# Kernel tuning notes

Hardware: AMD Instinct MI355X
Metric: run time of the kernel (lower is better)

Reference implementation:

```python
import jax, jax.numpy as jnp
import numpy as np

B, S, HID = 1, 4096, 2048
NH, NKV, HD, RD = 16, 4, 128, 64
EPS = 1e-6
SCALE = HD ** -0.5


def _rmsnorm(x, w, eps=EPS):
    x32 = x.astype(jnp.float32)
    var = jnp.mean(x32 * x32, axis=-1, keepdims=True)
    return (w * (x32 * jax.lax.rsqrt(var + eps))).astype(x.dtype)


def _rotate_half(x):
    x1, x2 = jnp.split(x, 2, axis=-1)
    return jnp.concatenate([-x2, x1], axis=-1)


def setup_inputs() -> dict:
    key = jax.random.key(0)
    ks = jax.random.split(key, 6)
    hidden_states = jax.random.normal(ks[0], (B, S, HID), dtype=jnp.float32)
    # real rotary embeddings for rotary_dim=RD
    inv_freq = 1.0 / (10000.0 ** (jnp.arange(0, RD, 2, dtype=jnp.float32) / RD))
    pos = jnp.arange(S, dtype=jnp.float32)
    freqs = pos[:, None] * inv_freq[None, :]          # [S, RD/2]
    emb = jnp.concatenate([freqs, freqs], axis=-1)     # [S, RD]
    cos = jnp.cos(emb)[None]                           # [1, S, RD]
    sin = jnp.sin(emb)[None]
    w = 0.02
    Wq = jax.random.normal(ks[1], (NH * HD, HID), dtype=jnp.float32) * w
    Wk = jax.random.normal(ks[2], (NKV * HD, HID), dtype=jnp.float32) * w
    Wv = jax.random.normal(ks[3], (NKV * HD, HID), dtype=jnp.float32) * w
    Wo = jax.random.normal(ks[4], (HID, NH * HD), dtype=jnp.float32) * w
    q_norm_w = jnp.ones((NH * HD,), dtype=jnp.float32)
    k_norm_w = jnp.ones((NKV * HD,), dtype=jnp.float32)
    return {"hidden_states": hidden_states, "cos": cos, "sin": sin,
            "Wq": Wq, "Wk": Wk, "Wv": Wv, "Wo": Wo,
            "q_norm_w": q_norm_w, "k_norm_w": k_norm_w}


def _attention(hidden_states, cos, sin, Wq, Wk, Wv, Wo, q_norm_w, k_norm_w):
    bsz, q_len, _ = hidden_states.shape
    q = hidden_states @ Wq.T                 # [B,S,NH*HD]
    k = hidden_states @ Wk.T                 # [B,S,NKV*HD]
    v = hidden_states @ Wv.T
    q = _rmsnorm(q, q_norm_w)
    k = _rmsnorm(k, k_norm_w)
    q = q.reshape(bsz, q_len, NH, HD).transpose(0, 2, 1, 3)   # b h s d
    k = k.reshape(bsz, q_len, NKV, HD).transpose(0, 2, 1, 3)
    v = v.reshape(bsz, q_len, NKV, HD).transpose(0, 2, 1, 3)
    # partial RoPE on first RD dims
    c = cos[:, None]  # [B,1,S,RD]
    s = sin[:, None]
    q_rot, q_pass = q[..., :RD], q[..., RD:]
    k_rot, k_pass = k[..., :RD], k[..., RD:]
    q = jnp.concatenate([q_rot * c + _rotate_half(q_rot) * s, q_pass], axis=-1)
    k = jnp.concatenate([k_rot * c + _rotate_half(k_rot) * s, k_pass], axis=-1)
    # GQA: repeat kv heads
    n_rep = NH // NKV
    k = jnp.repeat(k, n_rep, axis=1)
    v = jnp.repeat(v, n_rep, axis=1)
    scores = jnp.einsum('bhqd,bhkd->bhqk', q, k) * SCALE
    causal = jnp.triu(jnp.full((q_len, q_len), -jnp.inf, dtype=scores.dtype), k=1)
    scores = scores + causal
    probs = jax.nn.softmax(scores.astype(jnp.float32), axis=-1).astype(q.dtype)
    out = jnp.einsum('bhqk,bhkd->bhqd', probs, v)
    out = out.transpose(0, 2, 1, 3).reshape(bsz, q_len, NH * HD)
    return out @ Wo.T


def reference(hidden_states, cos, sin, Wq, Wk, Wv, Wo, q_norm_w, k_norm_w):
    return _attention(hidden_states, cos, sin, Wq, Wk, Wv, Wo, q_norm_w, k_norm_w)
```

## Files before the change

### kernel.cpp

```cpp
#include <hip/hip_runtime.h>

typedef unsigned short u16;
typedef unsigned int   u32;
typedef __bf16 bf16x8 __attribute__((ext_vector_type(8)));
typedef float  f32x4  __attribute__((ext_vector_type(4)));

#define S_LEN 4096
#define HIDN  2048
#define NHEAD 16
#define NKVH  4
#define HDIM  128
#define ROTD  64
#define QKVN  3072

__device__ __forceinline__ u16 f2bf(float f) {
  union { float f; u32 u; } v; v.f = f;
  u32 r = v.u + 0x7FFFu + ((v.u >> 16) & 1u);
  return (u16)(r >> 16);
}
__device__ __forceinline__ u16 f2bf_fast(float f) {
  union { __bf16 b; u16 u; } cv; cv.b = (__bf16)f; return cv.u;
}
__device__ __forceinline__ float bf2f(u16 u) {
  union { u32 u; float f; } v; v.u = ((u32)u) << 16; return v.f;
}
__device__ __forceinline__ void gl2lds16(const u16* g, u16* l) {
  __builtin_amdgcn_global_load_lds((const __attribute__((address_space(1))) void*)g,
                                   (__attribute__((address_space(3))) void*)l, 16, 0, 0);
}
__device__ __forceinline__ f32x4 mfma_bf16(bf16x8 a, bf16x8 b, f32x4 c) {
  return __builtin_amdgcn_mfma_f32_16x16x32_bf16(a, b, c, 0, 0, 0);
}
template <int N> __device__ __forceinline__ void vmwait() {
  if constexpr (N == 7)      asm volatile("s_waitcnt vmcnt(7)" ::: "memory");
  else if constexpr (N == 6) asm volatile("s_waitcnt vmcnt(6)" ::: "memory");
  else                       asm volatile("s_waitcnt vmcnt(0)" ::: "memory");
}

__global__ __launch_bounds__(256) void cvt_f32_bf16(const float* __restrict__ in,
                                                    u16* __restrict__ out) {
  size_t i = ((size_t)blockIdx.x * 256 + threadIdx.x) * 8;
  float4 a = *(const float4*)(in + i);
  float4 b = *(const float4*)(in + i + 4);
  uint4 r;
  r.x = (u32)f2bf(a.x) | ((u32)f2bf(a.y) << 16);
  r.y = (u32)f2bf(a.z) | ((u32)f2bf(a.w) << 16);
  r.z = (u32)f2bf(b.x) | ((u32)f2bf(b.y) << 16);
  r.w = (u32)f2bf(b.z) | ((u32)f2bf(b.w) << 16);
  *(uint4*)(out + i) = r;
}

template <int BN, int NB, bool BF16OUT>
__global__ __launch_bounds__(512, 2) void gemm_big(const u16* __restrict__ A,
                                                   const u16* __restrict__ Bm,
                                                   void* __restrict__ Cp,
                                                   int M, int N, int K) {
  constexpr int WNC = BN / 4;
  constexpr int NF  = WNC / 16;
  constexpr int ASZ = 256 * 128;
  constexpr int BUF = ASZ + BN * 128;
  constexpr int LOADS = 4 + NB;
  __shared__ __align__(1024) char lds[2 * BUF];

  const int tid = threadIdx.x, wave = tid >> 6, lane = tid & 63;
  const int wm = wave >> 2, wn = wave & 3;
  const int row0 = blockIdx.x * 256, col0 = blockIdx.y * BN;
  const int l8 = lane >> 3, l7 = lane & 7;
  const int T = K >> 6;

  const u16* gA[4]; const u16* gB[NB];
  u16* ldsA[4]; u16* ldsB[NB];
  #pragma unroll
  for (int i = 0; i < 4; ++i) {
    gA[i]  = A + (size_t)(row0 + wave * 32 + i * 8 + l8) * K + (l7 ^ l8) * 8;
    ldsA[i] = (u16*)(lds + wave * 4096 + i * 1024);
  }
  #pragma unroll
  for (int i = 0; i < NB; ++i) {
    gB[i]  = Bm + (size_t)(col0 + wave * (BN / 8) + i * 8 + l8) * K + (l7 ^ l8) * 8;
    ldsB[i] = (u16*)(lds + ASZ + wave * (BN * 16) + i * 1024);
  }
  auto stage = [&](int buf, int t) {
    const size_t ko = (size_t)t * 64;
    #pragma unroll
    for (int i = 0; i < 4; ++i)
      gl2lds16(gA[i] + ko, (u16*)((char*)ldsA[i] + buf * BUF));
    #pragma unroll
    for (int i = 0; i < NB; ++i)
      gl2lds16(gB[i] + ko, (u16*)((char*)ldsB[i] + buf * BUF));
  };

  const int colx0 = (((lane >> 4))     ^ l7) * 16;
  const int colx1 = ((4 + (lane >> 4)) ^ l7) * 16;
  const char* aB = lds + (wm * 128 + (lane & 15)) * 128;
  const char* bB = lds + ASZ + (wn * WNC + (lane & 15)) * 128;

  f32x4 acc[8][NF];
  #pragma unroll
  for (int i = 0; i < 8; ++i)
    #pragma unroll
    for (int j = 0; j < NF; ++j) { f32x4 z = {0.f,0.f,0.f,0.f}; acc[i][j] = z; }

  stage(0, 0);
  stage(1, 1);
  vmwait<LOADS>();
  __builtin_amdgcn_s_barrier();

  for (int t = 0; t < T; ++t) {
    const int bo = (t & 1) * BUF;
    #pragma unroll
    for (int kh = 0; kh < 2; ++kh) {
      const int cx = kh ? colx1 : colx0;
      bf16x8 bfr[NF];
      #pragma unroll
      for (int nf = 0; nf < NF; ++nf)
        bfr[nf] = *(const bf16x8*)(bB + bo + nf * 2048 + cx);
      #pragma unroll
      for (int mh = 0; mh < 2; ++mh) {
        bf16x8 af[4];
        #pragma unroll
        for (int mf = 0; mf < 4; ++mf)
          af[mf] = *(const bf16x8*)(aB + bo + mh * 8192 + mf * 2048 + cx);
        __builtin_amdgcn_s_setprio(1);
        #pragma unroll
        for (int mf = 0; mf < 4; ++mf)
          #pragma unroll
          for (int nf = 0; nf < NF; ++nf)
            acc[mh * 4 + mf][nf] = mfma_bf16(af[mf], bfr[nf], acc[mh * 4 + mf][nf]);
        __builtin_amdgcn_s_setprio(0);
      }
    }
    asm volatile("s_waitcnt lgkmcnt(0)" ::: "memory");
    __builtin_amdgcn_s_barrier();
    if (t + 2 < T) stage(t & 1, t + 2);
    if (t + 1 < T) {
      if (t + 2 < T) vmwait<LOADS>();
      else           vmwait<0>();
      __builtin_amdgcn_s_barrier();
    }
  }

  const int mwv = row0 + wm * 128, nwv = col0 + wn * WNC;
  #pragma unroll
  for (int mf8 = 0; mf8 < 8; ++mf8)
    #pragma unroll
    for (int nf = 0; nf < NF; ++nf)
      #pragma unroll
      for (int r = 0; r < 4; ++r) {
        int m = mwv + (mf8 >> 2) * 64 + (mf8 & 3) * 16 + (lane >> 4) * 4 + r;
        int n = nwv + nf * 16 + (lane & 15);
        float v = acc[mf8][nf][r];
        if (BF16OUT) ((u16*)Cp)[(size_t)m * N + n] = f2bf(v);
        else         ((float*)Cp)[(size_t)m * N + n] = v;
      }
}

__global__ __launch_bounds__(256) void norm_rope(const u16* __restrict__ qkv,
                                                 const float* __restrict__ cosb,
                                                 const float* __restrict__ sinb,
                                                 const float* __restrict__ qw,
                                                 const float* __restrict__ kw,
                                                 u16* __restrict__ Qo,
                                                 u16* __restrict__ Ko) {
  const int s = blockIdx.x, t = threadIdx.x;
  const int wave = t >> 6, lane = t & 63;
  const float SL = 0.08838834764831845f * 1.4426950408889634f;
  __shared__ float rowbuf[HIDN];
  __shared__ float red[4];
  const u16* base = qkv + (size_t)s * QKVN;

  float x[8];
  {
    uint4 v = *(const uint4*)(base + t * 8);
    u32 w4[4] = {v.x, v.y, v.z, v.w};
    #pragma unroll
    for (int j = 0; j < 4; ++j) {
      x[2*j]   = bf2f((u16)(w4[j] & 0xffffu));
      x[2*j+1] = bf2f((u16)(w4[j] >> 16));
    }
  }
  float ss = 0.f;
  #pragma unroll
  for (int j = 0; j < 8; ++j) ss += x[j] * x[j];
  #pragma unroll
  for (int m = 1; m < 64; m <<= 1) ss += __shfl_xor(ss, m);
  if (lane == 0) red[wave] = ss;
  __syncthreads();
  float rs = rsqrtf((red[0]+red[1]+red[2]+red[3]) * (1.0f / HIDN) + 1e-6f);
  #pragma unroll
  for (int j = 0; j < 8; ++j) rowbuf[t*8 + j] = x[j] * rs * qw[t*8 + j];
  __syncthreads();
  {
    int i0 = t * 8, d0 = i0 & (HDIM - 1), hh = i0 >> 7;
    float o[8];
    if (d0 < ROTD) {
      #pragma unroll
      for (int j = 0; j < 8; ++j) {
        int d = d0 + j;
        float rot = (d < 32) ? -rowbuf[i0 + j + 32] : rowbuf[i0 + j - 32];
        o[j] = rowbuf[i0 + j] * cosb[s*ROTD + d] + rot * sinb[s*ROTD + d];
      }
    } else {
      #pragma unroll
      for (int j = 0; j < 8; ++j) o[j] = rowbuf[i0 + j];
    }
    uint4 r;
    r.x = (u32)f2bf(o[0]*SL) | ((u32)f2bf(o[1]*SL) << 16);
    r.y = (u32)f2bf(o[2]*SL) | ((u32)f2bf(o[3]*SL) << 16);
    r.z = (u32)f2bf(o[4]*SL) | ((u32)f2bf(o[5]*SL) << 16);
    r.w = (u32)f2bf(o[6]*SL) | ((u32)f2bf(o[7]*SL) << 16);
    *(uint4*)(Qo + ((size_t)hh * S_LEN + s) * HDIM + d0) = r;
  }

  const u16* kbase = base + HIDN;
  float y0, y1;
  { u32 v = *(const u32*)(kbase + t * 2); y0 = bf2f((u16)(v & 0xffffu)); y1 = bf2f((u16)(v >> 16)); }
  float ss2 = y0*y0 + y1*y1;
  #pragma unroll
  for (int m = 1; m < 64; m <<= 1) ss2 += __shfl_xor(ss2, m);
  __syncthreads();
  if (lane == 0) red[wave] = ss2;
  __syncthreads();
  float rs2 = rsqrtf((red[0]+red[1]+red[2]+red[3]) * (1.0f / 512.0f) + 1e-6f);
  rowbuf[t*2]     = y0 * rs2 * kw[t*2];
  rowbuf[t*2 + 1] = y1 * rs2 * kw[t*2 + 1];
  __syncthreads();
  {
    int i0 = t * 2, d0 = i0 & (HDIM - 1), hh = i0 >> 7;
    float o0, o1;
    if (d0 < ROTD) {
      float r0 = (d0 < 32) ? -rowbuf[i0 + 32] : rowbuf[i0 - 32];
      float r1 = (d0 + 1 < 32) ? -rowbuf[i0 + 1 + 32] : rowbuf[i0 + 1 - 32];
      o0 = rowbuf[i0]     * cosb[s*ROTD + d0]     + r0 * sinb[s*ROTD + d0];
      o1 = rowbuf[i0 + 1] * cosb[s*ROTD + d0 + 1] + r1 * sinb[s*ROTD + d0 + 1];
    } else { o0 = rowbuf[i0]; o1 = rowbuf[i0 + 1]; }
    u32 r = (u32)f2bf(o0) | ((u32)f2bf(o1) << 16);
    *(u32*)(Ko + ((size_t)hh * S_LEN + s) * HDIM + d0) = r;
  }
}

__global__ __launch_bounds__(256) void vtrans(const u16* __restrict__ qkv,
                                              u16* __restrict__ Vt) {
  const int sb = blockIdx.x * 64, db = blockIdx.y * 64, kvh = blockIdx.z;
  __shared__ u16 tile[64][72];
  const int t = threadIdx.x;
  {
    int r = t >> 2, cc = (t & 3) * 16;
    const u16* src = qkv + (size_t)(sb + r) * QKVN + 2560 + kvh * HDIM + db + cc;
    *(uint4*)&tile[r][cc]     = *(const uint4*)(src);
    *(uint4*)&tile[r][cc + 8] = *(const uint4*)(src + 8);
  }
  __syncthreads();
  {
    int d = t >> 2, sc = (t & 3) * 16;
    u16 tmp[16];
    #pragma unroll
    for (int j = 0; j < 16; ++j) tmp[j] = tile[sc + j][d];
    u16* dst = Vt + ((size_t)kvh * HDIM + db + d) * S_LEN + sb + sc;
    *(uint4*)dst       = *(uint4*)&tmp[0];
    *(uint4*)(dst + 8) = *(uint4*)&tmp[8];
  }
}

__global__ __launch_bounds__(256, 2) void attn_fwd(const u16* __restrict__ Q,
                                                   const u16* __restrict__ K,
                                                   const u16* __restrict__ Vt,
                                                   u16* __restrict__ O) {
  const int bid  = blockIdx.x;
  const int slot = bid & 7, p = bid >> 3;
  const int kvh  = slot >> 1, hp = slot & 1;
  const int tid = threadIdx.x, wave = tid >> 6, lane = tid & 63;
  const int h  = kvh * 4 + hp * 2 + (wave >> 1);
  const int wq = wave & 1;
  __shared__ u16 Ks[2][64][128];
  __shared__ u16 Vs[2][128][64];
  __shared__ u16 Ps[4][32][64];

  const u16* gKb[4]; const u16* gVb[4];
  #pragma unroll
  for (int i = 0; i < 4; ++i) {
    int cc = wave * 4 + i;
    int rk = cc * 4 + (lane >> 4);
    gKb[i] = K + ((size_t)kvh * S_LEN + rk) * HDIM + ((lane & 15) ^ (rk & 7)) * 8;
    int rv = cc * 8 + (lane >> 3);
    gVb[i] = Vt + ((size_t)kvh * HDIM + rv) * S_LEN + ((lane & 7) ^ (rv & 7)) * 8;
  }
  auto stage = [&](int buf, int kvb) {
    #pragma unroll
    for (int i = 0; i < 4; ++i) {
      int cc = wave * 4 + i;
      gl2lds16(gKb[i] + (size_t)kvb * HDIM, &Ks[buf][cc * 4][0]);
      gl2lds16(gVb[i] + kvb,                &Vs[buf][cc * 8][0]);
    }
  };

  int offv[4];
  #pragma unroll
  for (int kk = 0; kk < 4; ++kk)
    offv[kk] = (kk * 64 + (lane >> 4) * 16) ^ ((lane & 7) << 4);
  const char* ksB = (const char*)Ks + (lane & 15) * 256;
  const char* vsB = (const char*)Vs + (lane & 15) * 128;
  const char* psB = (const char*)Ps + wave * 4096 + (lane & 15) * 128;
  char*       pwB = (char*)Ps + wave * 4096;
  const int   lx2 = (lane & 15) * 2;

  stage(0, 0);
  __syncthreads();
  int cur = 0;

  for (int job = 0; job < 2; ++job) {
    const int qb = job ? (63 - p) : p;
    const int ntiles = qb + 1;
    const int qg0 = qb * 64 + wq * 32 + (lane >> 4) * 4;

    bf16x8 qf[2][4];
    #pragma unroll
    for (int qm = 0; qm < 2; ++qm) {
      const u16* qptr = Q + ((size_t)h * S_LEN + qb * 64 + wq * 32 + qm * 16 + (lane & 15)) * HDIM
                        + (lane >> 4) * 8;
      #pragma unroll
      for (int kk = 0; kk < 4; ++kk) qf[qm][kk] = *(const bf16x8*)(qptr + kk * 32);
    }

    float lsum[2][4];
    #pragma unroll
    for (int qm = 0; qm < 2; ++qm)
      #pragma unroll
      for (int r = 0; r < 4; ++r) lsum[qm][r] = 0.f;
    f32x4 o[2][8];
    #pragma unroll
    for (int qm = 0; qm < 2; ++qm)
      #pragma unroll
      for (int i = 0; i < 8; ++i) { f32x4 z = {0.f,0.f,0.f,0.f}; o[qm][i] = z; }

    for (int kt = 0; kt < ntiles; ++kt) {
      if (kt + 1 < ntiles)      stage(cur ^ 1, (kt + 1) * 64);
      else if (job == 0)        stage(cur ^ 1, 0);

      const int bufo = cur << 14;

      f32x4 sc[2][4];
      #pragma unroll
      for (int qm = 0; qm < 2; ++qm)
        #pragma unroll
        for (int i = 0; i < 4; ++i) { f32x4 z = {0.f,0.f,0.f,0.f}; sc[qm][i] = z; }
      __builtin_amdgcn_s_setprio(1);
      #pragma unroll
      for (int kk = 0; kk < 4; ++kk)
        #pragma unroll
        for (int nf = 0; nf < 4; ++nf) {
          bf16x8 kf = *(const bf16x8*)(ksB + bufo + nf * 4096 + offv[kk]);
          sc[0][nf] = mfma_bf16(qf[0][kk], kf, sc[0][nf]);
          sc[1][nf] = mfma_bf16(qf[1][kk], kf, sc[1][nf]);
        }
      __builtin_amdgcn_s_setprio(0);

      if (kt == ntiles - 1) {
        const int kvb = kt * 64;
        #pragma unroll
        for (int qm = 0; qm < 2; ++qm)
          #pragma unroll
          for (int nf = 0; nf < 4; ++nf) {
            int col = kvb + nf * 16 + (lane & 15);
            #pragma unroll
            for (int r = 0; r < 4; ++r) {
              float e = __builtin_amdgcn_exp2f(sc[qm][nf][r]);
              e = (col <= qg0 + qm * 16 + r) ? e : 0.f;
              sc[qm][nf][r] = e;
              lsum[qm][r] += e;
            }
          }
      } else {
        #pragma unroll
        for (int qm = 0; qm < 2; ++qm)
          #pragma unroll
          for (int nf = 0; nf < 4; ++nf)
            #pragma unroll
            for (int r = 0; r < 4; ++r) {
              float e = __builtin_amdgcn_exp2f(sc[qm][nf][r]);
              sc[qm][nf][r] = e;
              lsum[qm][r] += e;
            }
      }

      #pragma unroll
      for (int qm = 0; qm < 2; ++qm)
        #pragma unroll
        for (int nf = 0; nf < 4; ++nf)
          #pragma unroll
          for (int r = 0; r < 4; ++r) {
            int prow = qm * 16 + (lane >> 4) * 4 + r;
            int bcol = (nf * 32 + lx2) ^ ((prow & 7) << 4);
            *(u16*)(pwB + prow * 128 + bcol) = f2bf_fast(sc[qm][nf][r]);
          }

      __builtin_amdgcn_s_setprio(1);
      #pragma unroll
      for (int ks = 0; ks < 2; ++ks) {
        bf16x8 pf0 = *(const bf16x8*)(psB + offv[ks]);
        bf16x8 pf1 = *(const bf16x8*)(psB + 2048 + offv[ks]);
        #pragma unroll
        for (int nf2 = 0; nf2 < 8; ++nf2) {
          bf16x8 vf = *(const bf16x8*)(vsB + bufo + nf2 * 2048 + offv[ks]);
          o[0][nf2] = mfma_bf16(pf0, vf, o[0][nf2]);
          o[1][nf2] = mfma_bf16(pf1, vf, o[1][nf2]);
        }
      }
      __builtin_amdgcn_s_setprio(0);

      __syncthreads();
      cur ^= 1;
    }

    #pragma unroll
    for (int qm = 0; qm < 2; ++qm)
      #pragma unroll
      for (int r = 0; r < 4; ++r) {
        float lt = lsum[qm][r];
        #pragma unroll
        for (int m = 1; m < 16; m <<= 1) lt += __shfl_xor(lt, m);
        float inv = 1.f / lt;
        int srow = qg0 + qm * 16 + r;
        #pragma unroll
        for (int nf2 = 0; nf2 < 8; ++nf2) {
          int col = h * HDIM + nf2 * 16 + (lane & 15);
          O[(size_t)srow * HIDN + col] = f2bf_fast(o[qm][nf2][r] * inv);
        }
      }
  }
}

extern "C" void kernel_launch(void* const* d_in, const int* in_sizes, int n_in,
                              void* d_out, int out_size, void* d_ws, size_t ws_size,
                              hipStream_t stream) {
  (void)in_sizes; (void)n_in; (void)out_size; (void)ws_size;
  const float* h    = (const float*)d_in[0];
  const float* cosb = (const float*)d_in[1];
  const float* sinb = (const float*)d_in[2];
  const float* Wq   = (const float*)d_in[3];
  const float* Wk   = (const float*)d_in[4];
  const float* Wv   = (const float*)d_in[5];
  const float* Wo   = (const float*)d_in[6];
  const float* qw   = (const float*)d_in[7];
  const float* kw   = (const float*)d_in[8];
  float* out = (float*)d_out;

  char* ws = (char*)d_ws;
  u16* hbf  = (u16*)(ws);
  u16* Kb   = (u16*)(ws + (16u << 20));
  u16* Vtb  = (u16*)(ws + (20u << 20));
  u16* wqkv = (u16*)(ws + (24u << 20));
  u16* Qb   = (u16*)(ws + (24u << 20));
  u16* qkvb = (u16*)(ws + (40u << 20));
  u16* wob  = (u16*)(ws + (40u << 20));

  cvt_f32_bf16<<<4096, 256, 0, stream>>>(h, hbf);
  cvt_f32_bf16<<<2048, 256, 0, stream>>>(Wq, wqkv);
  cvt_f32_bf16<<<512, 256, 0, stream>>>(Wk, wqkv + 4u * 1024 * 1024);
  cvt_f32_bf16<<<512, 256, 0, stream>>>(Wv, wqkv + 5u * 1024 * 1024);

  gemm_big<192, 3, true><<<dim3(16, 16), 512, 0, stream>>>(hbf, wqkv, qkvb,
                                                           4096, 3072, 2048);

  norm_rope<<<4096, 256, 0, stream>>>(qkvb, cosb, sinb, qw, kw, Qb, Kb);
  vtrans<<<dim3(64, 2, 4), 256, 0, stream>>>(qkvb, Vtb);

  cvt_f32_bf16<<<2048, 256, 0, stream>>>(Wo, wob);

  attn_fwd<<<dim3(256), 256, 0, stream>>>(Qb, Kb, Vtb, hbf);

  gemm_big<128, 2, false><<<dim3(16, 16), 512, 0, stream>>>(hbf, wob, out,
                                                            4096, 2048, 2048);
}
```

Measured before the change: 267.0 us.

## Split KV tile across wave pairs in attention, doubling grid to one head per block

```diff
diff --git a/kernel.cpp b/kernel.cpp
--- a/kernel.cpp
+++ b/kernel.cpp
@@ -266,15 +266,17 @@
                                                    const u16* __restrict__ K,
                                                    const u16* __restrict__ Vt,
                                                    u16* __restrict__ O) {
-  const int bid  = blockIdx.x;
-  const int slot = bid & 7, p = bid >> 3;
-  const int kvh  = slot >> 1, hp = slot & 1;
+  const int n    = blockIdx.x;
+  const int slot = n & 7, kq = n >> 3;
+  const int kvh  = slot >> 1;
+  const int h    = kvh * 4 + (slot & 1) * 2 + (kq & 1);
+  const int p    = kq >> 1;
   const int tid = threadIdx.x, wave = tid >> 6, lane = tid & 63;
-  const int h  = kvh * 4 + hp * 2 + (wave >> 1);
-  const int wq = wave & 1;
+  const int rh   = wave & 1;
+  const int kvh2 = wave >> 1;
   __shared__ u16 Ks[2][64][128];
   __shared__ u16 Vs[2][128][64];
-  __shared__ u16 Ps[4][32][64];
+  __shared__ u16 Ps[2][32][64];
 
   const u16* gKb[4]; const u16* gVb[4];
   #pragma unroll
@@ -298,11 +300,12 @@
   #pragma unroll
   for (int kk = 0; kk < 4; ++kk)
     offv[kk] = (kk * 64 + (lane >> 4) * 16) ^ ((lane & 7) << 4);
-  const char* ksB = (const char*)Ks + (lane & 15) * 256;
+  const char* ksB = (const char*)Ks + kvh2 * 8192 + (lane & 15) * 256;
   const char* vsB = (const char*)Vs + (lane & 15) * 128;
-  const char* psB = (const char*)Ps + wave * 4096 + (lane & 15) * 128;
-  char*       pwB = (char*)Ps + wave * 4096;
+  const char* psB = (const char*)Ps + rh * 4096 + (lane & 15) * 128;
+  char*       pwB = (char*)Ps + rh * 4096;
   const int   lx2 = (lane & 15) * 2;
+  const int   vko = offv[kvh2];
 
   stage(0, 0);
   __syncthreads();
@@ -311,12 +314,12 @@
   for (int job = 0; job < 2; ++job) {
     const int qb = job ? (63 - p) : p;
     const int ntiles = qb + 1;
-    const int qg0 = qb * 64 + wq * 32 + (lane >> 4) * 4;
+    const int qg0 = qb * 64 + rh * 32 + (lane >> 4) * 4;
 
     bf16x8 qf[2][4];
     #pragma unroll
     for (int qm = 0; qm < 2; ++qm) {
-      const u16* qptr = Q + ((size_t)h * S_LEN + qb * 64 + wq * 32 + qm * 16 + (lane & 15)) * HDIM
+      const u16* qptr = Q + ((size_t)h * S_LEN + qb * 64 + rh * 32 + qm * 16 + (lane & 15)) * HDIM
                         + (lane >> 4) * 8;
       #pragma unroll
       for (int kk = 0; kk < 4; ++kk) qf[qm][kk] = *(const bf16x8*)(qptr + kk * 32);
@@ -338,95 +341,128 @@
       else if (job == 0)        stage(cur ^ 1, 0);
 
       const int bufo = cur << 14;
-
-      f32x4 sc[2][4];
-      #pragma unroll
-      for (int qm = 0; qm < 2; ++qm)
-        #pragma unroll
-        for (int i = 0; i < 4; ++i) { f32x4 z = {0.f,0.f,0.f,0.f}; sc[qm][i] = z; }
-      __builtin_amdgcn_s_setprio(1);
-      #pragma unroll
-      for (int kk = 0; kk < 4; ++kk)
-        #pragma unroll
-        for (int nf = 0; nf < 4; ++nf) {
-          bf16x8 kf = *(const bf16x8*)(ksB + bufo + nf * 4096 + offv[kk]);
-          sc[0][nf] = mfma_bf16(qf[0][kk], kf, sc[0][nf]);
-          sc[1][nf] = mfma_bf16(qf[1][kk], kf, sc[1][nf]);
+      const bool diag = (kt == ntiles - 1);
+
+      if (!(diag && kvh2 == 1 && rh == 0)) {
+        f32x4 sc[2][2];
+        #pragma unroll
+        for (int qm = 0; qm < 2; ++qm)
+          #pragma unroll
+          for (int i = 0; i < 2; ++i) { f32x4 z = {0.f,0.f,0.f,0.f}; sc[qm][i] = z; }
+        __builtin_amdgcn_s_setprio(1);
+        #pragma unroll
+        for (int kk = 0; kk < 4; ++kk)
+          #pragma unroll
+          for (int nf = 0; nf < 2; ++nf) {
+            bf16x8 kf = *(const bf16x8*)(ksB + bufo + nf * 4096 + offv[kk]);
+            sc[0][nf] = mfma_bf16(qf[0][kk], kf, sc[0][nf]);
+            sc[1][nf] = mfma_bf16(qf[1][kk], kf, sc[1][nf]);
+          }
+        __builtin_amdgcn_s_setprio(0);
+
+        if (diag) {
+          const int kvb = kt * 64;
+          #pragma unroll
+          for (int qm = 0; qm < 2; ++qm)
+            #pragma unroll
+            for (int nf = 0; nf < 2; ++nf) {
+              int col = kvb + kvh2 * 32 + nf * 16 + (lane & 15);
+              #pragma unroll
+              for (int r = 0; r < 4; ++r) {
+                float e = __builtin_amdgcn_exp2f(sc[qm][nf][r]);
+                e = (col <= qg0 + qm * 16 + r) ? e : 0.f;
+                sc[qm][nf][r] = e;
+                lsum[qm][r] += e;
+              }
+            }
+        } else {
+          #pragma unroll
+          for (int qm = 0; qm < 2; ++qm)
+            #pragma unroll
+            for (int nf = 0; nf < 2; ++nf)
+              #pragma unroll
+              for (int r = 0; r < 4; ++r) {
+                float e = __builtin_amdgcn_exp2f(sc[qm][nf][r]);
+                sc[qm][nf][r] = e;
+                lsum[qm][r] += e;
+              }
         }
-      __builtin_amdgcn_s_setprio(0);
-
-      if (kt == ntiles - 1) {
-        const int kvb = kt * 64;
-        #pragma unroll
-        for (int qm = 0; qm < 2; ++qm)
-          #pragma unroll
-          for (int nf = 0; nf < 4; ++nf) {
-            int col = kvb + nf * 16 + (lane & 15);
+
+        #pragma unroll
+        for (int qm = 0; qm < 2; ++qm)
+          #pragma unroll
+          for (int nf = 0; nf < 2; ++nf)
             #pragma unroll
             for (int r = 0; r < 4; ++r) {
-              float e = __builtin_amdgcn_exp2f(sc[qm][nf][r]);
-              e = (col <= qg0 + qm * 16 + r) ? e : 0.f;
-              sc[qm][nf][r] = e;
-              lsum[qm][r] += e;
+              int prow = qm * 16 + (lane >> 4) * 4 + r;
+              int bcol = (kvh2 * 64 + nf * 32 + lx2) ^ ((prow & 7) << 4);
+              *(u16*)(pwB + prow * 128 + bcol) = f2bf_fast(sc[qm][nf][r]);
             }
-          }
-      } else {
-        #pragma unroll
-        for (int qm = 0; qm < 2; ++qm)
-          #pragma unroll
-          for (int nf = 0; nf < 4; ++nf)
-            #pragma unroll
-            for (int r = 0; r < 4; ++r) {
-              float e = __builtin_amdgcn_exp2f(sc[qm][nf][r]);
-              sc[qm][nf][r] = e;
-              lsum[qm][r] += e;
-            }
-      }
-
-      #pragma unroll
-      for (int qm = 0; qm < 2; ++qm)
-        #pragma unroll
-        for (int nf = 0; nf < 4; ++nf)
-          #pragma unroll
-          for (int r = 0; r < 4; ++r) {
-            int prow = qm * 16 + (lane >> 4) * 4 + r;
-            int bcol = (nf * 32 + lx2) ^ ((prow & 7) << 4);
-            *(u16*)(pwB + prow * 128 + bcol) = f2bf_fast(sc[qm][nf][r]);
-          }
-
-      __builtin_amdgcn_s_setprio(1);
-      #pragma unroll
-      for (int ks = 0; ks < 2; ++ks) {
-        bf16x8 pf0 = *(const bf16x8*)(psB + offv[ks]);
-        bf16x8 pf1 = *(const bf16x8*)(psB + 2048 + offv[ks]);
+
+        bf16x8 pf0, pf1;
+        pf0 = *(const bf16x8*)(psB + vko);
+        pf1 = *(const bf16x8*)(psB + 2048 + vko);
+        __builtin_amdgcn_s_setprio(1);
         #pragma unroll
         for (int nf2 = 0; nf2 < 8; ++nf2) {
-          bf16x8 vf = *(const bf16x8*)(vsB + bufo + nf2 * 2048 + offv[ks]);
+          bf16x8 vf = *(const bf16x8*)(vsB + bufo + nf2 * 2048 + vko);
           o[0][nf2] = mfma_bf16(pf0, vf, o[0][nf2]);
           o[1][nf2] = mfma_bf16(pf1, vf, o[1][nf2]);
         }
+        __builtin_amdgcn_s_setprio(0);
       }
-      __builtin_amdgcn_s_setprio(0);
 
       __syncthreads();
       cur ^= 1;
     }
 
-    #pragma unroll
-    for (int qm = 0; qm < 2; ++qm)
-      #pragma unroll
-      for (int r = 0; r < 4; ++r) {
-        float lt = lsum[qm][r];
-        #pragma unroll
-        for (int m = 1; m < 16; m <<= 1) lt += __shfl_xor(lt, m);
-        float inv = 1.f / lt;
-        int srow = qg0 + qm * 16 + r;
-        #pragma unroll
-        for (int nf2 = 0; nf2 < 8; ++nf2) {
-          int col = h * HDIM + nf2 * 16 + (lane & 15);
-          O[(size_t)srow * HIDN + col] = f2bf_fast(o[qm][nf2][r] * inv);
-        }
+    {
+      f32x4* scr = (f32x4*)((rh == 0) ? (char*)Ks + (cur ^ 1) * 16384
+                                      : (char*)Vs + (cur ^ 1) * 16384);
+      float* lsc = (float*)Ps;
+      if (kvh2 == 1) {
+        #pragma unroll
+        for (int qm = 0; qm < 2; ++qm)
+          #pragma unroll
+          for (int nf2 = 0; nf2 < 8; ++nf2)
+            scr[(qm * 8 + nf2) * 64 + lane] = o[qm][nf2];
+        #pragma unroll
+        for (int qm = 0; qm < 2; ++qm)
+          #pragma unroll
+          for (int r = 0; r < 4; ++r)
+            lsc[rh * 512 + (qm * 4 + r) * 64 + lane] = lsum[qm][r];
       }
+      __syncthreads();
+      if (kvh2 == 0) {
+        #pragma unroll
+        for (int qm = 0; qm < 2; ++qm)
+          #pragma unroll
+          for (int nf2 = 0; nf2 < 8; ++nf2)
+            o[qm][nf2] += scr[(qm * 8 + nf2) * 64 + lane];
+        #pragma unroll
+        for (int qm = 0; qm < 2; ++qm)
+          #pragma unroll
+          for (int r = 0; r < 4; ++r)
+            lsum[qm][r] += lsc[rh * 512 + (qm * 4 + r) * 64 + lane];
+
+        #pragma unroll
+        for (int qm = 0; qm < 2; ++qm)
+          #pragma unroll
+          for (int r = 0; r < 4; ++r) {
+            float lt = lsum[qm][r];
+            #pragma unroll
+            for (int m = 1; m < 16; m <<= 1) lt += __shfl_xor(lt, m);
+            float inv = 1.f / lt;
+            int srow = qg0 + qm * 16 + r;
+            #pragma unroll
+            for (int nf2 = 0; nf2 < 8; ++nf2) {
+              int col = h * HDIM + nf2 * 16 + (lane & 15);
+              O[(size_t)srow * HIDN + col] = f2bf_fast(o[qm][nf2][r] * inv);
+            }
+          }
+      }
+      __syncthreads();
+    }
   }
 }
 
@@ -467,7 +503,7 @@
 
   cvt_f32_bf16<<<2048, 256, 0, stream>>>(Wo, wob);
 
-  attn_fwd<<<dim3(256), 256, 0, stream>>>(Qb, Kb, Vtb, hbf);
+  attn_fwd<<<dim3(512), 256, 0, stream>>>(Qb, Kb, Vtb, hbf);
 
   gemm_big<128, 2, false><<<dim3(16, 16), 512, 0, stream>>>(hbf, wob, out,
                                                             4096, 2048, 2048);
```

After: 240.7 us. -9.9%, faster.
